# Kernel optimization log

Hardware: AMD Instinct MI355X
Metric: run time of the kernel (lower is better)

## Reference

```python
import jax, jax.numpy as jnp
import numpy as np

B, NQ, NKV = 16, 4096, 77
QUERY_DIM, CONTEXT_DIM = 320, 768
HEADS, DIM_HEAD = 8, 64
INNER = HEADS * DIM_HEAD
SCALE = DIM_HEAD ** (-0.5)
MAX_NEG = -jnp.finfo(jnp.float32).max / 2


def setup_inputs() -> dict:
    key = jax.random.key(0)
    ks = jax.random.split(key, 8)
    x = jax.random.normal(ks[0], (B, NQ, QUERY_DIM), dtype=jnp.float32)
    context = jax.random.normal(ks[1], (B, NKV, CONTEXT_DIM), dtype=jnp.float32)
    mask = jax.random.randint(ks[2], (B, 1, 1, NKV), 0, 2).astype(bool)
    s = 0.02
    Wq = jax.random.normal(ks[3], (QUERY_DIM, INNER), dtype=jnp.float32) * s
    Wk = jax.random.normal(ks[4], (CONTEXT_DIM, INNER), dtype=jnp.float32) * s
    Wv = jax.random.normal(ks[5], (CONTEXT_DIM, INNER), dtype=jnp.float32) * s
    Wo = jax.random.normal(ks[6], (INNER, QUERY_DIM), dtype=jnp.float32) * s
    bo = jnp.zeros((QUERY_DIM,), dtype=jnp.float32)
    return {"x": x, "context": context, "mask": mask,
            "Wq": Wq, "Wk": Wk, "Wv": Wv, "Wo": Wo, "bo": bo}


def reference(x, context, mask, Wq, Wk, Wv, Wo, bo):
    # projections (bias-free Linears)
    q = (x @ Wq).reshape(B, NQ, HEADS, DIM_HEAD)        # b q h d
    k = (context @ Wk).reshape(B, NKV, HEADS, DIM_HEAD)  # b k h d
    v = (context @ Wv).reshape(B, NKV, HEADS, DIM_HEAD)  # b k h d
    # additive mask bias: 0 where mask, -finfo.max/2 where ~mask (matches masked_fill_)
    bias = jnp.where(mask, jnp.float32(0), MAX_NEG)      # broadcast to b h q k
    sim = jnp.einsum('bqhd,bkhd->bhqk', q, k) * SCALE + bias
    attn = jax.nn.softmax(sim, axis=-1)
    out = jnp.einsum('bhqk,bkhd->bqhd', attn, v).reshape(B, NQ, INNER)
    return out @ Wo + bo  # dropout p=0 -> identity
```

## Files before the change

kernel.cpp:

```cpp
#include <hip/hip_runtime.h>

typedef unsigned short ushort_t;
typedef __attribute__((ext_vector_type(8))) short bf16x8;
typedef __attribute__((ext_vector_type(4))) float f32x4;

#define B_SZ   16
#define NQ     4096
#define NKV    77
#define QDIM   320
#define CDIM   768
#define HEADS  8
#define DHEAD  64
#define INNER  512
#define M_ROWS (B_SZ * NQ)
#define VT_STR 104

__device__ __forceinline__ ushort_t f2bf(float f) {
  unsigned u = __builtin_bit_cast(unsigned, f);
  u = (u + 0x7fffu + ((u >> 16) & 1u)) >> 16;
  return (ushort_t)u;
}

__device__ __forceinline__ void async16(const ushort_t* g, ushort_t* l) {
  __builtin_amdgcn_global_load_lds(
      (const __attribute__((address_space(1))) unsigned int*)g,
      (__attribute__((address_space(3))) unsigned int*)l,
      16, 0, 0);
}

__global__ void mask_bias_kernel(const unsigned char* __restrict__ mraw,
                                 float* __restrict__ biasT) {
  __shared__ int s_u8, s_w4;
  if (threadIdx.x == 0) { s_u8 = 0; s_w4 = 0; }
  __syncthreads();
  const int nbytes = B_SZ * NKV;
  for (int i = threadIdx.x; i < nbytes; i += blockDim.x) {
    unsigned char v = mraw[i];
    if (v && (i & 3)) atomicOr(&s_u8, 1);
    if (v && ((i & 7) == 4)) atomicOr(&s_w4, 1);
  }
  __syncthreads();
  int mode = s_u8 ? 0 : (s_w4 ? 1 : 2);
  for (int i = threadIdx.x; i < B_SZ * 80; i += blockDim.x) {
    int b = i / 80, kv = i - b * 80;
    float bias = -2e30f;
    if (kv < NKV) {
      int idx = b * NKV + kv;
      long long m;
      if (mode == 0)      m = (long long)mraw[idx];
      else if (mode == 1) m = (long long)((const int*)mraw)[idx];
      else                m = ((const long long*)mraw)[idx];
      bias = m ? 0.0f : -1e30f;
    }
    biasT[i] = bias;
  }
}

__global__ void cast_f32_bf16(const float* __restrict__ in,
                              ushort_t* __restrict__ out, int n4) {
  int i = blockIdx.x * blockDim.x + threadIdx.x;
  int stride = gridDim.x * blockDim.x;
  const float4* in4 = (const float4*)in;
  ushort4* out4 = (ushort4*)out;
  for (; i < n4; i += stride) {
    float4 v = in4[i];
    ushort4 o;
    o.x = f2bf(v.x); o.y = f2bf(v.y); o.z = f2bf(v.z); o.w = f2bf(v.w);
    out4[i] = o;
  }
}

__global__ void tcast_f32_bf16(const float* __restrict__ in,
                               ushort_t* __restrict__ out,
                               int K, int N, int Npad, float scale) {
  int i = blockIdx.x * blockDim.x + threadIdx.x;
  int stride = gridDim.x * blockDim.x;
  int total = Npad * K;
  for (; i < total; i += stride) {
    int n = i / K, k = i - n * K;
    out[i] = (n < N) ? f2bf(in[(size_t)k * N + n] * scale) : (ushort_t)0;
  }
}

__global__ void vtrans_kernel(const ushort_t* __restrict__ kvb,
                              ushort_t* __restrict__ vt) {
  const int h = blockIdx.y, b = blockIdx.z;
  const int wid = threadIdx.x >> 6, lane = threadIdx.x & 63;
  const int d = blockIdx.x * 4 + wid;
  ushort_t* dst = vt + (size_t)(b * HEADS + h) * (64 * VT_STR) + d * VT_STR;
  for (int kv = lane; kv < VT_STR; kv += 64)
    dst[kv] = (kv < NKV)
        ? kvb[(size_t)(b * NKV + kv) * 1024 + 512 + h * 64 + d]
        : (ushort_t)0;
}

__global__ __launch_bounds__(256) void gemm_bf16(
    const ushort_t* __restrict__ A, const ushort_t* __restrict__ Bt,
    ushort_t* __restrict__ Cb,
    int K, int Astride, int Bstride, int Cstride) {
  __shared__ ushort_t As[128 * 64];
  __shared__ ushort_t Bs[128 * 64];
  const int tid = threadIdx.x;
  const int wid = tid >> 6, lane = tid & 63;
  const int wr = wid >> 1, wc = wid & 1;
  const int tileM = blockIdx.x * 128, tileN = blockIdx.y * 128;

  f32x4 acc[4][4];
#pragma unroll
  for (int m = 0; m < 4; ++m)
#pragma unroll
    for (int n = 0; n < 4; ++n) acc[m][n] = (f32x4){0.f, 0.f, 0.f, 0.f};

  const int srow = lane >> 3;
  const int scol = (lane & 7) * 8;

  for (int kt = 0; kt < K; kt += 64) {
    __syncthreads();
#pragma unroll
    for (int j = 0; j < 4; ++j) {
      int s = wid * 4 + j;
      const ushort_t* ga = A + (size_t)(tileM + s * 8 + srow) * Astride + kt + scol;
      const ushort_t* gb = Bt + (size_t)(tileN + s * 8 + srow) * Bstride + kt + scol;
      async16(ga, As + s * 512);
      async16(gb, Bs + s * 512);
    }
    __syncthreads();
#pragma unroll
    for (int kc = 0; kc < 2; ++kc) {
      bf16x8 af[4], bfr[4];
#pragma unroll
      for (int m = 0; m < 4; ++m)
        af[m] = *(const bf16x8*)&As[(wr * 64 + m * 16 + (lane & 15)) * 64 + kc * 32 + (lane >> 4) * 8];
#pragma unroll
      for (int n = 0; n < 4; ++n)
        bfr[n] = *(const bf16x8*)&Bs[(wc * 64 + n * 16 + (lane & 15)) * 64 + kc * 32 + (lane >> 4) * 8];
#pragma unroll
      for (int m = 0; m < 4; ++m)
#pragma unroll
        for (int n = 0; n < 4; ++n)
          acc[m][n] = __builtin_amdgcn_mfma_f32_16x16x32_bf16(af[m], bfr[n], acc[m][n], 0, 0, 0);
    }
  }

  const int r0 = tileM + wr * 64;
  const int c0 = tileN + wc * 64;
  const int rl2 = (lane >> 4) * 4;
  const int cl = lane & 15;
#pragma unroll
  for (int m = 0; m < 4; ++m)
#pragma unroll
    for (int n = 0; n < 4; ++n) {
      int col = c0 + n * 16 + cl;
#pragma unroll
      for (int r = 0; r < 4; ++r)
        Cb[(size_t)(r0 + m * 16 + rl2 + r) * Cstride + col] = f2bf(acc[m][n][r]);
    }
}

__global__ __launch_bounds__(256, 2) void gemm_qproj_ws(
    const float* __restrict__ x, const ushort_t* __restrict__ Wt,
    ushort_t* __restrict__ qb) {
  __shared__ __align__(16) float As[32 * 320];
  const int tid = threadIdx.x, wid = tid >> 6, lane = tid & 63;
  const int rl = lane & 15, g = lane >> 4;
  const int nbase = blockIdx.y * 128 + wid * 32;
  const size_t Mbase = (size_t)blockIdx.x * 128;

  bf16x8 bf[2][10];
#pragma unroll
  for (int n = 0; n < 2; ++n)
#pragma unroll
    for (int kc = 0; kc < 10; ++kc)
      bf[n][kc] = *(const bf16x8*)&Wt[(size_t)(nbase + n * 16 + rl) * QDIM + kc * 32 + g * 8];

  unsigned off[10];
#pragma unroll
  for (int i = 0; i < 10; ++i) {
    unsigned p = wid * 10240 + i * 1024 + lane * 16;
    unsigned row = p / 1280u;
    unsigned rem = p - row * 1280u;
    off[i] = (unsigned)((Mbase + row) * 1280u) + (rem ^ ((row & 7u) << 4));
  }

  const char* xB = (const char*)x;
  char* AsB = (char*)As;

  for (int it = 0; it < 4; ++it) {
#pragma unroll
    for (int i = 0; i < 10; ++i)
      async16((const ushort_t*)(xB + off[i]),
              (ushort_t*)(AsB + wid * 10240 + i * 1024));
    __syncthreads();

    f32x4 acc[2][2];
#pragma unroll
    for (int m = 0; m < 2; ++m)
#pragma unroll
      for (int n = 0; n < 2; ++n) acc[m][n] = (f32x4){0.f, 0.f, 0.f, 0.f};

#pragma unroll
    for (int kc = 0; kc < 10; ++kc) {
      bf16x8 af[2];
#pragma unroll
      for (int m = 0; m < 2; ++m) {
        const int row = m * 16 + rl;
        const int cb = kc * 128 + g * 32;
        const int s = (row & 7) << 4;
        f32x4 lo = *(const f32x4*)(AsB + row * 1280 + (cb ^ s));
        f32x4 hi = *(const f32x4*)(AsB + row * 1280 + ((cb + 16) ^ s));
        unsigned w0, w1, w2, w3;
        asm("v_cvt_pk_bf16_f32 %0, %1, %2" : "=v"(w0) : "v"(lo[0]), "v"(lo[1]));
        asm("v_cvt_pk_bf16_f32 %0, %1, %2" : "=v"(w1) : "v"(lo[2]), "v"(lo[3]));
        asm("v_cvt_pk_bf16_f32 %0, %1, %2" : "=v"(w2) : "v"(hi[0]), "v"(hi[1]));
        asm("v_cvt_pk_bf16_f32 %0, %1, %2" : "=v"(w3) : "v"(hi[2]), "v"(hi[3]));
        union { unsigned u[4]; bf16x8 v; } cv;
        cv.u[0] = w0; cv.u[1] = w1; cv.u[2] = w2; cv.u[3] = w3;
        af[m] = cv.v;
      }
#pragma unroll
      for (int m = 0; m < 2; ++m)
#pragma unroll
        for (int n = 0; n < 2; ++n)
          acc[m][n] = __builtin_amdgcn_mfma_f32_16x16x32_bf16(af[m], bf[n][kc], acc[m][n], 0, 0, 0);
    }

    const size_t r0 = Mbase + it * 32;
#pragma unroll
    for (int m = 0; m < 2; ++m)
#pragma unroll
      for (int n = 0; n < 2; ++n) {
        const int col = nbase + n * 16 + rl;
#pragma unroll
        for (int r = 0; r < 4; ++r)
          qb[(r0 + m * 16 + g * 4 + r) * INNER + col] = f2bf(acc[m][n][r]);
      }

    if (it < 3) {
      __syncthreads();
#pragma unroll
      for (int i = 0; i < 10; ++i) off[i] += 32 * 1280;
    }
  }
}

__global__ __launch_bounds__(512, 2) void gemm_oproj(
    const ushort_t* __restrict__ A, const ushort_t* __restrict__ Wt,
    const float* __restrict__ bo, float* __restrict__ out) {
  __shared__ ushort_t As[2][128 * 64];
  __shared__ ushort_t Bs[2][384 * 64];
  const int tid = threadIdx.x;
  const int wid = tid >> 6, lane = tid & 63;
  const int wr = wid & 1, wc = wid >> 1;
  const int rl = lane & 15, kh = (lane >> 4) * 8;
  const int tileM = blockIdx.x * 128;

  f32x4 acc[4][6];
#pragma unroll
  for (int m = 0; m < 4; ++m)
#pragma unroll
    for (int n = 0; n < 6; ++n) acc[m][n] = (f32x4){0.f, 0.f, 0.f, 0.f};

#define OP_STAGE(BUF, KT)                                                     \
  _Pragma("unroll")                                                           \
  for (int i = 0; i < 2; ++i) {                                               \
    int chunk = tid + i * 512;                                                \
    int row = chunk >> 3, c8 = chunk & 7;                                     \
    async16(A + (size_t)(tileM + row) * INNER + (KT) + c8 * 8,                \
            &As[BUF][chunk * 8]);                                             \
  }                                                                           \
  _Pragma("unroll")                                                           \
  for (int i = 0; i < 6; ++i) {                                               \
    int chunk = tid + i * 512;                                                \
    int n = chunk >> 3, c8 = chunk & 7;                                       \
    async16(Wt + (size_t)n * INNER + (KT) + c8 * 8, &Bs[BUF][chunk * 8]);     \
  }

  OP_STAGE(0, 0)
  __syncthreads();

  for (int s = 0; s < 8; ++s) {
    const int cur = s & 1;
    if (s < 7) { OP_STAGE(cur ^ 1, (s + 1) * 64) }
#pragma unroll
    for (int kc = 0; kc < 2; ++kc) {
      bf16x8 af[4], bfr[6];
#pragma unroll
      for (int m = 0; m < 4; ++m)
        af[m] = *(const bf16x8*)&As[cur][(wr * 64 + m * 16 + rl) * 64 + kc * 32 + kh];
#pragma unroll
      for (int n = 0; n < 6; ++n)
        bfr[n] = *(const bf16x8*)&Bs[cur][(wc * 96 + n * 16 + rl) * 64 + kc * 32 + kh];
#pragma unroll
      for (int m = 0; m < 4; ++m)
#pragma unroll
        for (int n = 0; n < 6; ++n)
          acc[m][n] = __builtin_amdgcn_mfma_f32_16x16x32_bf16(af[m], bfr[n], acc[m][n], 0, 0, 0);
    }
    __syncthreads();
  }

  const int r0 = tileM + wr * 64;
  const int c0 = wc * 96;
  const int rl2 = (lane >> 4) * 4, cl = lane & 15;
#pragma unroll
  for (int n = 0; n < 6; ++n) {
    int col = c0 + n * 16 + cl;
    if (col < QDIM) {
      float bv = bo[col];
#pragma unroll
      for (int m = 0; m < 4; ++m)
#pragma unroll
        for (int r = 0; r < 4; ++r)
          out[(size_t)(r0 + m * 16 + rl2 + r) * QDIM + col] = acc[m][n][r] + bv;
    }
  }
}

__global__ __launch_bounds__(256) void attn_kernel(
    const ushort_t* __restrict__ qb, const ushort_t* __restrict__ kvb,
    const ushort_t* __restrict__ vt, const float* __restrict__ biasT,
    ushort_t* __restrict__ ab) {
  __shared__ ushort_t Vt[64 * VT_STR];
  __shared__ ushort_t P[4 * 16 * VT_STR];
  const int qt = blockIdx.x, h = blockIdx.y, b = blockIdx.z;
  const int tid = threadIdx.x, wid = tid >> 6, lane = tid & 63;
  const int rl = lane & 15;
  const int kh = (lane >> 4) * 8;

  const ushort_t* vtg = vt + (size_t)(b * HEADS + h) * (64 * VT_STR);
  for (int i = tid; i < 832; i += 256) async16(vtg + i * 8, Vt + i * 8);
  for (int i = tid; i < 832; i += 256)
    *(bf16x8*)&P[i * 8] = (bf16x8){0, 0, 0, 0, 0, 0, 0, 0};

  bf16x8 kf[5][2];
  float bias_v[5];
#pragma unroll
  for (int nt = 0; nt < 5; ++nt) {
    int kv = nt * 16 + rl;
    bias_v[nt] = biasT[b * 80 + kv];
    kf[nt][0] = (bf16x8){0, 0, 0, 0, 0, 0, 0, 0};
    kf[nt][1] = (bf16x8){0, 0, 0, 0, 0, 0, 0, 0};
    if (kv < NKV) {
      const ushort_t* kp = &kvb[(size_t)(b * NKV + kv) * 1024 + h * 64 + kh];
      kf[nt][0] = *(const bf16x8*)kp;
      kf[nt][1] = *(const bf16x8*)(kp + 32);
    }
  }
  __syncthreads();

  const int qbase = b * NQ + qt * 256;
  const int pbase = wid * (16 * VT_STR);
#pragma unroll 1
  for (int chunk = 0; chunk < 4; ++chunk) {
    if (chunk) __syncthreads();
    const int row0 = chunk * 64 + wid * 16;

    const ushort_t* qp = &qb[(size_t)(qbase + row0 + rl) * INNER + h * 64 + kh];
    bf16x8 qf0 = *(const bf16x8*)qp;
    bf16x8 qf1 = *(const bf16x8*)(qp + 32);

    f32x4 s[5];
#pragma unroll
    for (int nt = 0; nt < 5; ++nt) {
      s[nt] = (f32x4){0.f, 0.f, 0.f, 0.f};
      s[nt] = __builtin_amdgcn_mfma_f32_16x16x32_bf16(qf0, kf[nt][0], s[nt], 0, 0, 0);
      s[nt] = __builtin_amdgcn_mfma_f32_16x16x32_bf16(qf1, kf[nt][1], s[nt], 0, 0, 0);
    }

    float mx[4] = {-3.0e38f, -3.0e38f, -3.0e38f, -3.0e38f};
#pragma unroll
    for (int nt = 0; nt < 5; ++nt)
#pragma unroll
      for (int r = 0; r < 4; ++r) {
        float v = s[nt][r] + bias_v[nt];
        s[nt][r] = v;
        mx[r] = fmaxf(mx[r], v);
      }
#pragma unroll
    for (int d = 1; d < 16; d <<= 1)
#pragma unroll
      for (int r = 0; r < 4; ++r) mx[r] = fmaxf(mx[r], __shfl_xor(mx[r], d, 64));

    float sm[4] = {0.f, 0.f, 0.f, 0.f};
#pragma unroll
    for (int nt = 0; nt < 5; ++nt)
#pragma unroll
      for (int r = 0; r < 4; ++r) {
        float p = __expf(s[nt][r] - mx[r]);
        s[nt][r] = p;
        sm[r] += p;
      }
#pragma unroll
    for (int d = 1; d < 16; d <<= 1)
#pragma unroll
      for (int r = 0; r < 4; ++r) sm[r] += __shfl_xor(sm[r], d, 64);

    float rcp[4];
#pragma unroll
    for (int r = 0; r < 4; ++r) rcp[r] = 1.0f / sm[r];

#pragma unroll
    for (int nt = 0; nt < 5; ++nt)
#pragma unroll
      for (int r = 0; r < 4; ++r)
        P[pbase + ((lane >> 4) * 4 + r) * VT_STR + nt * 16 + rl] = f2bf(s[nt][r]);

    f32x4 o[4];
#pragma unroll
    for (int n = 0; n < 4; ++n) o[n] = (f32x4){0.f, 0.f, 0.f, 0.f};
#pragma unroll
    for (int kc = 0; kc < 3; ++kc) {
      bf16x8 pf = *(const bf16x8*)&P[pbase + rl * VT_STR + kc * 32 + kh];
#pragma unroll
      for (int n = 0; n < 4; ++n) {
        bf16x8 vf = *(const bf16x8*)&Vt[(n * 16 + rl) * VT_STR + kc * 32 + kh];
        o[n] = __builtin_amdgcn_mfma_f32_16x16x32_bf16(pf, vf, o[n], 0, 0, 0);
      }
    }

#pragma unroll
    for (int n = 0; n < 4; ++n)
#pragma unroll
      for (int r = 0; r < 4; ++r)
        P[pbase + ((lane >> 4) * 4 + r) * VT_STR + n * 16 + rl] = f2bf(o[n][r] * rcp[r]);

    __syncthreads();

    {
      const int rflat = tid >> 2, d0 = (tid & 3) * 16;
      const ushort_t* src = &P[(rflat >> 4) * (16 * VT_STR) + (rflat & 15) * VT_STR + d0];
      ushort_t* dst = &ab[(size_t)(qbase + chunk * 64 + rflat) * INNER + h * 64 + d0];
      *(bf16x8*)dst = *(const bf16x8*)src;
      *(bf16x8*)(dst + 8) = *(const bf16x8*)(src + 8);
    }
  }
}

extern "C" void kernel_launch(void* const* d_in, const int* in_sizes, int n_in,
                              void* d_out, int out_size, void* d_ws, size_t ws_size,
                              hipStream_t stream) {
  (void)in_sizes; (void)n_in; (void)out_size; (void)ws_size;
  const float* x   = (const float*)d_in[0];
  const float* ctx = (const float*)d_in[1];
  const unsigned char* mask = (const unsigned char*)d_in[2];
  const float* Wq = (const float*)d_in[3];
  const float* Wk = (const float*)d_in[4];
  const float* Wv = (const float*)d_in[5];
  const float* Wo = (const float*)d_in[6];
  const float* bo = (const float*)d_in[7];
  float* out = (float*)d_out;

  char* ws = (char*)d_ws;
  size_t off = 0;
  auto alloc = [&](size_t bytes) {
    char* p = ws + off;
    off += (bytes + 255) & ~(size_t)255;
    return p;
  };
  float*    biasT = (float*)alloc(B_SZ * 80 * sizeof(float));
  ushort_t* ab    = (ushort_t*)alloc((size_t)M_ROWS * INNER * 2);
  ushort_t* qb    = (ushort_t*)alloc((size_t)M_ROWS * INNER * 2);
  ushort_t* cb    = (ushort_t*)alloc((size_t)1280 * CDIM * 2);
  ushort_t* Wqb   = (ushort_t*)alloc((size_t)INNER * QDIM * 2);
  ushort_t* Wkvb  = (ushort_t*)alloc((size_t)1024 * CDIM * 2);
  ushort_t* Wob   = (ushort_t*)alloc((size_t)384 * INNER * 2);
  ushort_t* kvb   = (ushort_t*)alloc((size_t)1280 * 1024 * 2);
  ushort_t* vt    = (ushort_t*)alloc((size_t)B_SZ * HEADS * 64 * VT_STR * 2);

  mask_bias_kernel<<<1, 256, 0, stream>>>(mask, biasT);
  cast_f32_bf16<<<512, 256, 0, stream>>>(ctx, cb, B_SZ * NKV * CDIM / 4);
  tcast_f32_bf16<<<640, 256, 0, stream>>>(Wq, Wqb, QDIM, INNER, INNER, 0.125f);
  tcast_f32_bf16<<<1536, 256, 0, stream>>>(Wk, Wkvb, CDIM, INNER, INNER, 1.0f);
  tcast_f32_bf16<<<1536, 256, 0, stream>>>(Wv, Wkvb + (size_t)INNER * CDIM, CDIM, INNER, INNER, 1.0f);
  tcast_f32_bf16<<<768, 256, 0, stream>>>(Wo, Wob, INNER, QDIM, 384, 1.0f);

  gemm_qproj_ws<<<dim3(M_ROWS / 128, 4), 256, 0, stream>>>(x, Wqb, qb);
  dim3 g2(1280 / 128, 1024 / 128);
  gemm_bf16<<<g2, 256, 0, stream>>>(cb, Wkvb, kvb, CDIM, CDIM, CDIM, 1024);
  vtrans_kernel<<<dim3(16, HEADS, B_SZ), 256, 0, stream>>>(kvb, vt);
  attn_kernel<<<dim3(NQ / 256, HEADS, B_SZ), 256, 0, stream>>>(qb, kvb, vt, biasT, ab);
  gemm_oproj<<<M_ROWS / 128, 512, 0, stream>>>(ab, Wob, bo, out);
}
```

Measured before the change: 210.6 us.

## Rewrite Q and output projection GEMMs with triple-buffered async LDS pipelines

The Q projection now uses 512-thread blocks that each cover a full 128x512 output tile. It streams x and Wq in K-chunks through a three-stage async global-to-LDS pipeline with explicit vmcnt waits and swizzled layouts, and stages the bf16 results through LDS so they can be written to global memory in coalesced 16-byte chunks. The output projection gets a similar three-stage pipeline with 32-wide K steps and XOR-swizzled LDS, replacing its previous double buffer. The aim is to hide global-load latency, avoid LDS bank conflicts and re-read x only once per tile. In exchange, large dynamic shared memory allocations (144KB and 96KB) reduce occupancy, and it relies on hand-tuned vmcnt counts.

New measurement: 190.8 us. -9.4%, faster.

```diff
diff --git a/kernel.cpp b/kernel.cpp
--- a/kernel.cpp
+++ b/kernel.cpp
@@ -27,6 +27,8 @@
       (__attribute__((address_space(3))) unsigned int*)l,
       16, 0, 0);
 }
+
+#define VMCNT(N) asm volatile("s_waitcnt vmcnt(" #N ")" ::: "memory")
 
 __global__ void mask_bias_kernel(const unsigned char* __restrict__ mraw,
                                  float* __restrict__ biasT) {
@@ -157,102 +159,142 @@
     }
 }
 
-__global__ __launch_bounds__(256, 2) void gemm_qproj_ws(
+__global__ __launch_bounds__(512, 2) void gemm_qproj_p(
     const float* __restrict__ x, const ushort_t* __restrict__ Wt,
     ushort_t* __restrict__ qb) {
-  __shared__ __align__(16) float As[32 * 320];
+  extern __shared__ char sm[];
   const int tid = threadIdx.x, wid = tid >> 6, lane = tid & 63;
   const int rl = lane & 15, g = lane >> 4;
-  const int nbase = blockIdx.y * 128 + wid * 32;
+  const int wr = wid & 1, wc = wid >> 1;
   const size_t Mbase = (size_t)blockIdx.x * 128;
 
-  bf16x8 bf[2][10];
-#pragma unroll
-  for (int n = 0; n < 2; ++n)
-#pragma unroll
-    for (int kc = 0; kc < 10; ++kc)
-      bf[n][kc] = *(const bf16x8*)&Wt[(size_t)(nbase + n * 16 + rl) * QDIM + kc * 32 + g * 8];
-
-  unsigned off[10];
-#pragma unroll
-  for (int i = 0; i < 10; ++i) {
-    unsigned p = wid * 10240 + i * 1024 + lane * 16;
-    unsigned row = p / 1280u;
-    unsigned rem = p - row * 1280u;
-    off[i] = (unsigned)((Mbase + row) * 1280u) + (rem ^ ((row & 7u) << 4));
-  }
-
+  size_t asrc[2]; unsigned adst[2];
+#pragma unroll
+  for (int i = 0; i < 2; ++i) {
+    int c = tid + i * 512, row = c >> 3, c16 = c & 7;
+    asrc[i] = (Mbase + row) * 1280 + (unsigned)((c16 * 16) ^ ((row & 7) << 4));
+    adst[i] = c * 16;
+  }
+  size_t bsrc[4]; unsigned bdst[4];
+#pragma unroll
+  for (int i = 0; i < 4; ++i) {
+    int c = tid + i * 512, row = c >> 2, c16 = c & 3;
+    bsrc[i] = (size_t)row * 640 + (unsigned)((c16 * 16) ^ ((row & 3) << 4));
+    bdst[i] = 16384 + c * 16;
+  }
   const char* xB = (const char*)x;
-  char* AsB = (char*)As;
-
-  for (int it = 0; it < 4; ++it) {
-#pragma unroll
-    for (int i = 0; i < 10; ++i)
-      async16((const ushort_t*)(xB + off[i]),
-              (ushort_t*)(AsB + wid * 10240 + i * 1024));
+  const char* WtB = (const char*)Wt;
+
+  f32x4 acc[4][8];
+#pragma unroll
+  for (int m = 0; m < 4; ++m)
+#pragma unroll
+    for (int n = 0; n < 8; ++n) acc[m][n] = (f32x4){0.f, 0.f, 0.f, 0.f};
+
+#define QSTAGE(K)                                                           \
+  {                                                                         \
+    char* bb = sm + (unsigned)((K) % 3) * 49152u;                           \
+    _Pragma("unroll")                                                       \
+    for (int i = 0; i < 2; ++i)                                             \
+      async16((const ushort_t*)(xB + asrc[i] + (size_t)(K) * 128),          \
+              (ushort_t*)(bb + adst[i]));                                   \
+    _Pragma("unroll")                                                       \
+    for (int i = 0; i < 4; ++i)                                             \
+      async16((const ushort_t*)(WtB + bsrc[i] + (size_t)(K) * 64),          \
+              (ushort_t*)(bb + bdst[i]));                                   \
+  }
+
+  QSTAGE(0)
+  QSTAGE(1)
+  for (int s = 0; s < 10; ++s) {
+    if (s < 8) QSTAGE(s + 2)
+    if (s < 8)       { VMCNT(12); }
+    else if (s == 8) { VMCNT(6); }
+    else             { VMCNT(0); }
+    __builtin_amdgcn_sched_barrier(0);
+    __builtin_amdgcn_s_barrier();
+    __builtin_amdgcn_sched_barrier(0);
+
+    const char* Ab = sm + (unsigned)(s % 3) * 49152u;
+    const char* Bb = Ab + 16384;
+    bf16x8 af[4], bfr[8];
+#pragma unroll
+    for (int m = 0; m < 4; ++m) {
+      const int row = wr * 64 + m * 16 + rl;
+      const int sw = (row & 7) << 4;
+      f32x4 lo = *(const f32x4*)(Ab + row * 128 + ((g * 32) ^ sw));
+      f32x4 hi = *(const f32x4*)(Ab + row * 128 + ((g * 32 + 16) ^ sw));
+      unsigned w0, w1, w2, w3;
+      asm("v_cvt_pk_bf16_f32 %0, %1, %2" : "=v"(w0) : "v"(lo[0]), "v"(lo[1]));
+      asm("v_cvt_pk_bf16_f32 %0, %1, %2" : "=v"(w1) : "v"(lo[2]), "v"(lo[3]));
+      asm("v_cvt_pk_bf16_f32 %0, %1, %2" : "=v"(w2) : "v"(hi[0]), "v"(hi[1]));
+      asm("v_cvt_pk_bf16_f32 %0, %1, %2" : "=v"(w3) : "v"(hi[2]), "v"(hi[3]));
+      union { unsigned u[4]; bf16x8 v; } cv;
+      cv.u[0] = w0; cv.u[1] = w1; cv.u[2] = w2; cv.u[3] = w3;
+      af[m] = cv.v;
+    }
+#pragma unroll
+    for (int n = 0; n < 8; ++n) {
+      const int row = wc * 128 + n * 16 + rl;
+      bfr[n] = *(const bf16x8*)(Bb + row * 64 + ((g * 16) ^ ((row & 3) << 4)));
+    }
+#pragma unroll
+    for (int m = 0; m < 4; ++m)
+#pragma unroll
+      for (int n = 0; n < 8; ++n)
+        acc[m][n] = __builtin_amdgcn_mfma_f32_16x16x32_bf16(af[m], bfr[n], acc[m][n], 0, 0, 0);
+    __builtin_amdgcn_sched_barrier(0);
+    __builtin_amdgcn_s_barrier();
+    __builtin_amdgcn_sched_barrier(0);
+  }
+
+  ushort_t* eb = (ushort_t*)sm;
+#pragma unroll
+  for (int h = 0; h < 2; ++h) {
+    if (h) __syncthreads();
+    if (wr == h) {
+#pragma unroll
+      for (int m = 0; m < 4; ++m)
+#pragma unroll
+        for (int n = 0; n < 8; ++n)
+#pragma unroll
+          for (int r = 0; r < 4; ++r)
+            eb[(m * 16 + g * 4 + r) * 512 + wc * 128 + n * 16 + rl] = f2bf(acc[m][n][r]);
+    }
     __syncthreads();
-
-    f32x4 acc[2][2];
-#pragma unroll
-    for (int m = 0; m < 2; ++m)
-#pragma unroll
-      for (int n = 0; n < 2; ++n) acc[m][n] = (f32x4){0.f, 0.f, 0.f, 0.f};
-
-#pragma unroll
-    for (int kc = 0; kc < 10; ++kc) {
-      bf16x8 af[2];
-#pragma unroll
-      for (int m = 0; m < 2; ++m) {
-        const int row = m * 16 + rl;
-        const int cb = kc * 128 + g * 32;
-        const int s = (row & 7) << 4;
-        f32x4 lo = *(const f32x4*)(AsB + row * 1280 + (cb ^ s));
-        f32x4 hi = *(const f32x4*)(AsB + row * 1280 + ((cb + 16) ^ s));
-        unsigned w0, w1, w2, w3;
-        asm("v_cvt_pk_bf16_f32 %0, %1, %2" : "=v"(w0) : "v"(lo[0]), "v"(lo[1]));
-        asm("v_cvt_pk_bf16_f32 %0, %1, %2" : "=v"(w1) : "v"(lo[2]), "v"(lo[3]));
-        asm("v_cvt_pk_bf16_f32 %0, %1, %2" : "=v"(w2) : "v"(hi[0]), "v"(hi[1]));
-        asm("v_cvt_pk_bf16_f32 %0, %1, %2" : "=v"(w3) : "v"(hi[2]), "v"(hi[3]));
-        union { unsigned u[4]; bf16x8 v; } cv;
-        cv.u[0] = w0; cv.u[1] = w1; cv.u[2] = w2; cv.u[3] = w3;
-        af[m] = cv.v;
-      }
-#pragma unroll
-      for (int m = 0; m < 2; ++m)
-#pragma unroll
-        for (int n = 0; n < 2; ++n)
-          acc[m][n] = __builtin_amdgcn_mfma_f32_16x16x32_bf16(af[m], bf[n][kc], acc[m][n], 0, 0, 0);
-    }
-
-    const size_t r0 = Mbase + it * 32;
-#pragma unroll
-    for (int m = 0; m < 2; ++m)
-#pragma unroll
-      for (int n = 0; n < 2; ++n) {
-        const int col = nbase + n * 16 + rl;
-#pragma unroll
-        for (int r = 0; r < 4; ++r)
-          qb[(r0 + m * 16 + g * 4 + r) * INNER + col] = f2bf(acc[m][n][r]);
-      }
-
-    if (it < 3) {
-      __syncthreads();
-#pragma unroll
-      for (int i = 0; i < 10; ++i) off[i] += 32 * 1280;
-    }
-  }
-}
-
-__global__ __launch_bounds__(512, 2) void gemm_oproj(
+#pragma unroll
+    for (int i = 0; i < 8; ++i) {
+      int c = tid + i * 512, row = c >> 6;
+      *(bf16x8*)(qb + (Mbase + h * 64 + row) * 512 + (c & 63) * 8) =
+          *(const bf16x8*)(eb + c * 8);
+    }
+  }
+}
+
+__global__ __launch_bounds__(512, 2) void gemm_oproj_p(
     const ushort_t* __restrict__ A, const ushort_t* __restrict__ Wt,
     const float* __restrict__ bo, float* __restrict__ out) {
-  __shared__ ushort_t As[2][128 * 64];
-  __shared__ ushort_t Bs[2][384 * 64];
-  const int tid = threadIdx.x;
-  const int wid = tid >> 6, lane = tid & 63;
+  extern __shared__ char sm[];
+  const int tid = threadIdx.x, wid = tid >> 6, lane = tid & 63;
+  const int rl = lane & 15, g = lane >> 4;
   const int wr = wid & 1, wc = wid >> 1;
-  const int rl = lane & 15, kh = (lane >> 4) * 8;
-  const int tileM = blockIdx.x * 128;
+  const size_t Mbase = (size_t)blockIdx.x * 128;
+
+  size_t asrc; unsigned adst;
+  {
+    int c = tid, row = c >> 2, c16 = c & 3;
+    asrc = (Mbase + row) * 1024 + (unsigned)((c16 * 16) ^ ((row & 3) << 4));
+    adst = c * 16;
+  }
+  size_t bsrc[3]; unsigned bdst[3];
+#pragma unroll
+  for (int i = 0; i < 3; ++i) {
+    int c = tid + i * 512, row = c >> 2, c16 = c & 3;
+    bsrc[i] = (size_t)row * 1024 + (unsigned)((c16 * 16) ^ ((row & 3) << 4));
+    bdst[i] = 8192 + c * 16;
+  }
+  const char* AB = (const char*)A;
+  const char* WtB = (const char*)Wt;
 
   f32x4 acc[4][6];
 #pragma unroll
@@ -260,58 +302,63 @@
 #pragma unroll
     for (int n = 0; n < 6; ++n) acc[m][n] = (f32x4){0.f, 0.f, 0.f, 0.f};
 
-#define OP_STAGE(BUF, KT)                                                     \
-  _Pragma("unroll")                                                           \
-  for (int i = 0; i < 2; ++i) {                                               \
-    int chunk = tid + i * 512;                                                \
-    int row = chunk >> 3, c8 = chunk & 7;                                     \
-    async16(A + (size_t)(tileM + row) * INNER + (KT) + c8 * 8,                \
-            &As[BUF][chunk * 8]);                                             \
-  }                                                                           \
-  _Pragma("unroll")                                                           \
-  for (int i = 0; i < 6; ++i) {                                               \
-    int chunk = tid + i * 512;                                                \
-    int n = chunk >> 3, c8 = chunk & 7;                                       \
-    async16(Wt + (size_t)n * INNER + (KT) + c8 * 8, &Bs[BUF][chunk * 8]);     \
-  }
-
-  OP_STAGE(0, 0)
-  __syncthreads();
-
-  for (int s = 0; s < 8; ++s) {
-    const int cur = s & 1;
-    if (s < 7) { OP_STAGE(cur ^ 1, (s + 1) * 64) }
-#pragma unroll
-    for (int kc = 0; kc < 2; ++kc) {
-      bf16x8 af[4], bfr[6];
-#pragma unroll
-      for (int m = 0; m < 4; ++m)
-        af[m] = *(const bf16x8*)&As[cur][(wr * 64 + m * 16 + rl) * 64 + kc * 32 + kh];
+#define OSTAGE(K)                                                           \
+  {                                                                         \
+    char* bb = sm + (unsigned)((K) % 3) * 32768u;                           \
+    async16((const ushort_t*)(AB + asrc + (size_t)(K) * 64),                \
+            (ushort_t*)(bb + adst));                                        \
+    _Pragma("unroll")                                                       \
+    for (int i = 0; i < 3; ++i)                                             \
+      async16((const ushort_t*)(WtB + bsrc[i] + (size_t)(K) * 64),          \
+              (ushort_t*)(bb + bdst[i]));                                   \
+  }
+
+  OSTAGE(0)
+  OSTAGE(1)
+  for (int s = 0; s < 16; ++s) {
+    if (s < 14) OSTAGE(s + 2)
+    if (s < 14)       { VMCNT(8); }
+    else if (s == 14) { VMCNT(4); }
+    else              { VMCNT(0); }
+    __builtin_amdgcn_sched_barrier(0);
+    __builtin_amdgcn_s_barrier();
+    __builtin_amdgcn_sched_barrier(0);
+
+    const char* Ab = sm + (unsigned)(s % 3) * 32768u;
+    const char* Bb = Ab + 8192;
+    bf16x8 af[4], bfr[6];
+#pragma unroll
+    for (int m = 0; m < 4; ++m) {
+      const int row = wr * 64 + m * 16 + rl;
+      af[m] = *(const bf16x8*)(Ab + row * 64 + ((g * 16) ^ ((row & 3) << 4)));
+    }
+#pragma unroll
+    for (int n = 0; n < 6; ++n) {
+      const int row = wc * 96 + n * 16 + rl;
+      bfr[n] = *(const bf16x8*)(Bb + row * 64 + ((g * 16) ^ ((row & 3) << 4)));
+    }
+#pragma unroll
+    for (int m = 0; m < 4; ++m)
 #pragma unroll
       for (int n = 0; n < 6; ++n)
-        bfr[n] = *(const bf16x8*)&Bs[cur][(wc * 96 + n * 16 + rl) * 64 + kc * 32 + kh];
-#pragma unroll
-      for (int m = 0; m < 4; ++m)
-#pragma unroll
-        for (int n = 0; n < 6; ++n)
-          acc[m][n] = __builtin_amdgcn_mfma_f32_16x16x32_bf16(af[m], bfr[n], acc[m][n], 0, 0, 0);
-    }
-    __syncthreads();
-  }
-
-  const int r0 = tileM + wr * 64;
+        acc[m][n] = __builtin_amdgcn_mfma_f32_16x16x32_bf16(af[m], bfr[n], acc[m][n], 0, 0, 0);
+    __builtin_amdgcn_sched_barrier(0);
+    __builtin_amdgcn_s_barrier();
+    __builtin_amdgcn_sched_barrier(0);
+  }
+
+  const size_t r0 = Mbase + wr * 64;
   const int c0 = wc * 96;
-  const int rl2 = (lane >> 4) * 4, cl = lane & 15;
 #pragma unroll
   for (int n = 0; n < 6; ++n) {
-    int col = c0 + n * 16 + cl;
+    int col = c0 + n * 16 + rl;
     if (col < QDIM) {
       float bv = bo[col];
 #pragma unroll
       for (int m = 0; m < 4; ++m)
 #pragma unroll
         for (int r = 0; r < 4; ++r)
-          out[(size_t)(r0 + m * 16 + rl2 + r) * QDIM + col] = acc[m][n][r] + bv;
+          out[(r0 + m * 16 + g * 4 + r) * QDIM + col] = acc[m][n][r] + bv;
     }
   }
 }
@@ -381,23 +428,23 @@
 #pragma unroll
       for (int r = 0; r < 4; ++r) mx[r] = fmaxf(mx[r], __shfl_xor(mx[r], d, 64));
 
-    float sm[4] = {0.f, 0.f, 0.f, 0.f};
+    float sm_[4] = {0.f, 0.f, 0.f, 0.f};
 #pragma unroll
     for (int nt = 0; nt < 5; ++nt)
 #pragma unroll
       for (int r = 0; r < 4; ++r) {
         float p = __expf(s[nt][r] - mx[r]);
         s[nt][r] = p;
-        sm[r] += p;
+        sm_[r] += p;
       }
 #pragma unroll
     for (int d = 1; d < 16; d <<= 1)
 #pragma unroll
-      for (int r = 0; r < 4; ++r) sm[r] += __shfl_xor(sm[r], d, 64);
+      for (int r = 0; r < 4; ++r) sm_[r] += __shfl_xor(sm_[r], d, 64);
 
     float rcp[4];
 #pragma unroll
-    for (int r = 0; r < 4; ++r) rcp[r] = 1.0f / sm[r];
+    for (int r = 0; r < 4; ++r) rcp[r] = 1.0f / sm_[r];
 
 #pragma unroll
     for (int nt = 0; nt < 5; ++nt)
@@ -449,6 +496,11 @@
   const float* Wo = (const float*)d_in[6];
   const float* bo = (const float*)d_in[7];
   float* out = (float*)d_out;
+
+  hipFuncSetAttribute((const void*)gemm_qproj_p,
+                      hipFuncAttributeMaxDynamicSharedMemorySize, 147456);
+  hipFuncSetAttribute((const void*)gemm_oproj_p,
+                      hipFuncAttributeMaxDynamicSharedMemorySize, 98304);
 
   char* ws = (char*)d_ws;
   size_t off = 0;
@@ -474,10 +526,10 @@
   tcast_f32_bf16<<<1536, 256, 0, stream>>>(Wv, Wkvb + (size_t)INNER * CDIM, CDIM, INNER, INNER, 1.0f);
   tcast_f32_bf16<<<768, 256, 0, stream>>>(Wo, Wob, INNER, QDIM, 384, 1.0f);
 
-  gemm_qproj_ws<<<dim3(M_ROWS / 128, 4), 256, 0, stream>>>(x, Wqb, qb);
+  gemm_qproj_p<<<M_ROWS / 128, 512, 147456, stream>>>(x, Wqb, qb);
   dim3 g2(1280 / 128, 1024 / 128);
   gemm_bf16<<<g2, 256, 0, stream>>>(cb, Wkvb, kvb, CDIM, CDIM, CDIM, 1024);
   vtrans_kernel<<<dim3(16, HEADS, B_SZ), 256, 0, stream>>>(kvb, vt);
   attn_kernel<<<dim3(NQ / 256, HEADS, B_SZ), 256, 0, stream>>>(qb, kvb, vt, biasT, ab);
-  gemm_oproj<<<M_ROWS / 128, 512, 0, stream>>>(ab, Wob, bo, out);
-}
+  gemm_oproj_p<<<M_ROWS / 128, 512, 98304, stream>>>(ab, Wob, bo, out);
+}
```

## Restructure Q and output projections into single-shot 64-row tiles with LDS-staged epilogue

Applied to the files above, without the earlier changes.

The Q projection now loads a 64x320 fp32 tile of x into LDS once, computes all 512 output columns per block with 8 waves, and stages results through LDS so global stores are coalesced 16-byte writes. The output projection loads the whole 64x512 A tile into swizzled LDS in one shot and reads Wo fragments directly from global/L2 instead of double-buffering both operands through LDS. Both cut per-block synchronisation and redundant A loads, at the cost of large dynamic LDS (80KB/64KB) per block, which may limit occupancy, and more global B-fragment traffic.

Result: slower. 293.9 us (+39.6%).

```diff
diff --git a/kernel.cpp b/kernel.cpp
--- a/kernel.cpp
+++ b/kernel.cpp
@@ -157,161 +157,133 @@
     }
 }
 
-__global__ __launch_bounds__(256, 2) void gemm_qproj_ws(
+__global__ __launch_bounds__(512, 2) void gemm_qproj_v3(
     const float* __restrict__ x, const ushort_t* __restrict__ Wt,
     ushort_t* __restrict__ qb) {
-  __shared__ __align__(16) float As[32 * 320];
+  extern __shared__ char sm[];
   const int tid = threadIdx.x, wid = tid >> 6, lane = tid & 63;
   const int rl = lane & 15, g = lane >> 4;
-  const int nbase = blockIdx.y * 128 + wid * 32;
-  const size_t Mbase = (size_t)blockIdx.x * 128;
-
-  bf16x8 bf[2][10];
-#pragma unroll
-  for (int n = 0; n < 2; ++n)
-#pragma unroll
-    for (int kc = 0; kc < 10; ++kc)
-      bf[n][kc] = *(const bf16x8*)&Wt[(size_t)(nbase + n * 16 + rl) * QDIM + kc * 32 + g * 8];
-
-  unsigned off[10];
+  const int wr = wid & 1, wc = wid >> 1;
+  const size_t Mbase = (size_t)blockIdx.x * 64;
+  const char* xB = (const char*)x;
+
 #pragma unroll
   for (int i = 0; i < 10; ++i) {
-    unsigned p = wid * 10240 + i * 1024 + lane * 16;
-    unsigned row = p / 1280u;
-    unsigned rem = p - row * 1280u;
-    off[i] = (unsigned)((Mbase + row) * 1280u) + (rem ^ ((row & 7u) << 4));
-  }
-
-  const char* xB = (const char*)x;
-  char* AsB = (char*)As;
-
-  for (int it = 0; it < 4; ++it) {
-#pragma unroll
-    for (int i = 0; i < 10; ++i)
-      async16((const ushort_t*)(xB + off[i]),
-              (ushort_t*)(AsB + wid * 10240 + i * 1024));
-    __syncthreads();
-
-    f32x4 acc[2][2];
+    unsigned c = tid + i * 512;
+    unsigned row = c / 80u, c16 = c - row * 80u;
+    size_t src = (Mbase + row) * 1280 + (size_t)((c16 ^ (row & 7u)) * 16);
+    async16((const ushort_t*)(xB + src), (ushort_t*)(sm + c * 16));
+  }
+  __syncthreads();
+
+  f32x4 acc[2][8];
+#pragma unroll
+  for (int m = 0; m < 2; ++m)
+#pragma unroll
+    for (int n = 0; n < 8; ++n) acc[m][n] = (f32x4){0.f, 0.f, 0.f, 0.f};
+
+#pragma unroll
+  for (int kc = 0; kc < 10; ++kc) {
+    bf16x8 bfr[8];
+#pragma unroll
+    for (int n = 0; n < 8; ++n)
+      bfr[n] = *(const bf16x8*)&Wt[(size_t)(wc * 128 + n * 16 + rl) * QDIM + kc * 32 + g * 8];
+    bf16x8 af[2];
+#pragma unroll
+    for (int m = 0; m < 2; ++m) {
+      const int row = wr * 32 + m * 16 + rl;
+      const int sw = (row & 7) << 4;
+      f32x4 lo = *(const f32x4*)(sm + row * 1280 + ((kc * 128 + g * 32) ^ sw));
+      f32x4 hi = *(const f32x4*)(sm + row * 1280 + ((kc * 128 + g * 32 + 16) ^ sw));
+      unsigned w0, w1, w2, w3;
+      asm("v_cvt_pk_bf16_f32 %0, %1, %2" : "=v"(w0) : "v"(lo[0]), "v"(lo[1]));
+      asm("v_cvt_pk_bf16_f32 %0, %1, %2" : "=v"(w1) : "v"(lo[2]), "v"(lo[3]));
+      asm("v_cvt_pk_bf16_f32 %0, %1, %2" : "=v"(w2) : "v"(hi[0]), "v"(hi[1]));
+      asm("v_cvt_pk_bf16_f32 %0, %1, %2" : "=v"(w3) : "v"(hi[2]), "v"(hi[3]));
+      union { unsigned u[4]; bf16x8 v; } cv;
+      cv.u[0] = w0; cv.u[1] = w1; cv.u[2] = w2; cv.u[3] = w3;
+      af[m] = cv.v;
+    }
 #pragma unroll
     for (int m = 0; m < 2; ++m)
 #pragma unroll
-      for (int n = 0; n < 2; ++n) acc[m][n] = (f32x4){0.f, 0.f, 0.f, 0.f};
-
-#pragma unroll
-    for (int kc = 0; kc < 10; ++kc) {
-      bf16x8 af[2];
-#pragma unroll
-      for (int m = 0; m < 2; ++m) {
-        const int row = m * 16 + rl;
-        const int cb = kc * 128 + g * 32;
-        const int s = (row & 7) << 4;
-        f32x4 lo = *(const f32x4*)(AsB + row * 1280 + (cb ^ s));
-        f32x4 hi = *(const f32x4*)(AsB + row * 1280 + ((cb + 16) ^ s));
-        unsigned w0, w1, w2, w3;
-        asm("v_cvt_pk_bf16_f32 %0, %1, %2" : "=v"(w0) : "v"(lo[0]), "v"(lo[1]));
-        asm("v_cvt_pk_bf16_f32 %0, %1, %2" : "=v"(w1) : "v"(lo[2]), "v"(lo[3]));
-        asm("v_cvt_pk_bf16_f32 %0, %1, %2" : "=v"(w2) : "v"(hi[0]), "v"(hi[1]));
-        asm("v_cvt_pk_bf16_f32 %0, %1, %2" : "=v"(w3) : "v"(hi[2]), "v"(hi[3]));
-        union { unsigned u[4]; bf16x8 v; } cv;
-        cv.u[0] = w0; cv.u[1] = w1; cv.u[2] = w2; cv.u[3] = w3;
-        af[m] = cv.v;
-      }
-#pragma unroll
-      for (int m = 0; m < 2; ++m)
-#pragma unroll
-        for (int n = 0; n < 2; ++n)
-          acc[m][n] = __builtin_amdgcn_mfma_f32_16x16x32_bf16(af[m], bf[n][kc], acc[m][n], 0, 0, 0);
-    }
-
-    const size_t r0 = Mbase + it * 32;
-#pragma unroll
-    for (int m = 0; m < 2; ++m)
-#pragma unroll
-      for (int n = 0; n < 2; ++n) {
-        const int col = nbase + n * 16 + rl;
-#pragma unroll
-        for (int r = 0; r < 4; ++r)
-          qb[(r0 + m * 16 + g * 4 + r) * INNER + col] = f2bf(acc[m][n][r]);
-      }
-
-    if (it < 3) {
-      __syncthreads();
-#pragma unroll
-      for (int i = 0; i < 10; ++i) off[i] += 32 * 1280;
-    }
-  }
-}
-
-__global__ __launch_bounds__(512, 2) void gemm_oproj(
+      for (int n = 0; n < 8; ++n)
+        acc[m][n] = __builtin_amdgcn_mfma_f32_16x16x32_bf16(af[m], bfr[n], acc[m][n], 0, 0, 0);
+  }
+
+  __syncthreads();
+  ushort_t* eb = (ushort_t*)sm;
+#pragma unroll
+  for (int m = 0; m < 2; ++m)
+#pragma unroll
+    for (int n = 0; n < 8; ++n)
+#pragma unroll
+      for (int r = 0; r < 4; ++r)
+        eb[(wr * 32 + m * 16 + g * 4 + r) * 528 + wc * 128 + n * 16 + rl] = f2bf(acc[m][n][r]);
+  __syncthreads();
+#pragma unroll
+  for (int i = 0; i < 8; ++i) {
+    unsigned flat = tid + i * 512;
+    unsigned row = flat >> 6, c8 = flat & 63;
+    *(bf16x8*)(qb + (Mbase + row) * INNER + c8 * 8) =
+        *(const bf16x8*)(sm + row * 1056 + c8 * 16);
+  }
+}
+
+__global__ __launch_bounds__(512, 2) void gemm_oproj_v3(
     const ushort_t* __restrict__ A, const ushort_t* __restrict__ Wt,
     const float* __restrict__ bo, float* __restrict__ out) {
-  __shared__ ushort_t As[2][128 * 64];
-  __shared__ ushort_t Bs[2][384 * 64];
-  const int tid = threadIdx.x;
-  const int wid = tid >> 6, lane = tid & 63;
+  extern __shared__ char sm[];
+  const int tid = threadIdx.x, wid = tid >> 6, lane = tid & 63;
+  const int rl = lane & 15, g = lane >> 4;
   const int wr = wid & 1, wc = wid >> 1;
-  const int rl = lane & 15, kh = (lane >> 4) * 8;
-  const int tileM = blockIdx.x * 128;
-
-  f32x4 acc[4][6];
-#pragma unroll
-  for (int m = 0; m < 4; ++m)
+  const size_t Mbase = (size_t)blockIdx.x * 64;
+  const char* AB = (const char*)A;
+
+#pragma unroll
+  for (int i = 0; i < 8; ++i) {
+    unsigned c = tid + i * 512;
+    unsigned row = c >> 6, c16 = c & 63;
+    size_t src = (Mbase + row) * 1024 + (size_t)((c16 ^ (row & 7u)) * 16);
+    async16((const ushort_t*)(AB + src), (ushort_t*)(sm + c * 16));
+  }
+  __syncthreads();
+
+  f32x4 acc[2][6];
+#pragma unroll
+  for (int m = 0; m < 2; ++m)
 #pragma unroll
     for (int n = 0; n < 6; ++n) acc[m][n] = (f32x4){0.f, 0.f, 0.f, 0.f};
 
-#define OP_STAGE(BUF, KT)                                                     \
-  _Pragma("unroll")                                                           \
-  for (int i = 0; i < 2; ++i) {                                               \
-    int chunk = tid + i * 512;                                                \
-    int row = chunk >> 3, c8 = chunk & 7;                                     \
-    async16(A + (size_t)(tileM + row) * INNER + (KT) + c8 * 8,                \
-            &As[BUF][chunk * 8]);                                             \
-  }                                                                           \
-  _Pragma("unroll")                                                           \
-  for (int i = 0; i < 6; ++i) {                                               \
-    int chunk = tid + i * 512;                                                \
-    int n = chunk >> 3, c8 = chunk & 7;                                       \
-    async16(Wt + (size_t)n * INNER + (KT) + c8 * 8, &Bs[BUF][chunk * 8]);     \
-  }
-
-  OP_STAGE(0, 0)
-  __syncthreads();
-
-  for (int s = 0; s < 8; ++s) {
-    const int cur = s & 1;
-    if (s < 7) { OP_STAGE(cur ^ 1, (s + 1) * 64) }
-#pragma unroll
-    for (int kc = 0; kc < 2; ++kc) {
-      bf16x8 af[4], bfr[6];
-#pragma unroll
-      for (int m = 0; m < 4; ++m)
-        af[m] = *(const bf16x8*)&As[cur][(wr * 64 + m * 16 + rl) * 64 + kc * 32 + kh];
+#pragma unroll 4
+  for (int kc = 0; kc < 16; ++kc) {
+    bf16x8 bfr[6];
+#pragma unroll
+    for (int n = 0; n < 6; ++n)
+      bfr[n] = *(const bf16x8*)&Wt[(size_t)(wc * 96 + n * 16 + rl) * INNER + kc * 32 + g * 8];
+    bf16x8 af[2];
+#pragma unroll
+    for (int m = 0; m < 2; ++m) {
+      const int row = wr * 32 + m * 16 + rl;
+      af[m] = *(const bf16x8*)(sm + row * 1024 + ((kc * 64 + g * 16) ^ ((row & 7) << 4)));
+    }
+#pragma unroll
+    for (int m = 0; m < 2; ++m)
 #pragma unroll
       for (int n = 0; n < 6; ++n)
-        bfr[n] = *(const bf16x8*)&Bs[cur][(wc * 96 + n * 16 + rl) * 64 + kc * 32 + kh];
-#pragma unroll
-      for (int m = 0; m < 4; ++m)
-#pragma unroll
-        for (int n = 0; n < 6; ++n)
-          acc[m][n] = __builtin_amdgcn_mfma_f32_16x16x32_bf16(af[m], bfr[n], acc[m][n], 0, 0, 0);
-    }
-    __syncthreads();
-  }
-
-  const int r0 = tileM + wr * 64;
-  const int c0 = wc * 96;
-  const int rl2 = (lane >> 4) * 4, cl = lane & 15;
+        acc[m][n] = __builtin_amdgcn_mfma_f32_16x16x32_bf16(af[m], bfr[n], acc[m][n], 0, 0, 0);
+  }
+
 #pragma unroll
   for (int n = 0; n < 6; ++n) {
-    int col = c0 + n * 16 + cl;
+    int col = wc * 96 + n * 16 + rl;
     if (col < QDIM) {
       float bv = bo[col];
 #pragma unroll
-      for (int m = 0; m < 4; ++m)
+      for (int m = 0; m < 2; ++m)
 #pragma unroll
         for (int r = 0; r < 4; ++r)
-          out[(size_t)(r0 + m * 16 + rl2 + r) * QDIM + col] = acc[m][n][r] + bv;
+          out[(Mbase + wr * 32 + m * 16 + g * 4 + r) * QDIM + col] = acc[m][n][r] + bv;
     }
   }
 }
@@ -381,23 +353,23 @@
 #pragma unroll
       for (int r = 0; r < 4; ++r) mx[r] = fmaxf(mx[r], __shfl_xor(mx[r], d, 64));
 
-    float sm[4] = {0.f, 0.f, 0.f, 0.f};
+    float sm_[4] = {0.f, 0.f, 0.f, 0.f};
 #pragma unroll
     for (int nt = 0; nt < 5; ++nt)
 #pragma unroll
       for (int r = 0; r < 4; ++r) {
         float p = __expf(s[nt][r] - mx[r]);
         s[nt][r] = p;
-        sm[r] += p;
+        sm_[r] += p;
       }
 #pragma unroll
     for (int d = 1; d < 16; d <<= 1)
 #pragma unroll
-      for (int r = 0; r < 4; ++r) sm[r] += __shfl_xor(sm[r], d, 64);
+      for (int r = 0; r < 4; ++r) sm_[r] += __shfl_xor(sm_[r], d, 64);
 
     float rcp[4];
 #pragma unroll
-    for (int r = 0; r < 4; ++r) rcp[r] = 1.0f / sm[r];
+    for (int r = 0; r < 4; ++r) rcp[r] = 1.0f / sm_[r];
 
 #pragma unroll
     for (int nt = 0; nt < 5; ++nt)
@@ -449,6 +421,11 @@
   const float* Wo = (const float*)d_in[6];
   const float* bo = (const float*)d_in[7];
   float* out = (float*)d_out;
+
+  hipFuncSetAttribute((const void*)gemm_qproj_v3,
+                      hipFuncAttributeMaxDynamicSharedMemorySize, 81920);
+  hipFuncSetAttribute((const void*)gemm_oproj_v3,
+                      hipFuncAttributeMaxDynamicSharedMemorySize, 65536);
 
   char* ws = (char*)d_ws;
   size_t off = 0;
@@ -474,10 +451,10 @@
   tcast_f32_bf16<<<1536, 256, 0, stream>>>(Wv, Wkvb + (size_t)INNER * CDIM, CDIM, INNER, INNER, 1.0f);
   tcast_f32_bf16<<<768, 256, 0, stream>>>(Wo, Wob, INNER, QDIM, 384, 1.0f);
 
-  gemm_qproj_ws<<<dim3(M_ROWS / 128, 4), 256, 0, stream>>>(x, Wqb, qb);
+  gemm_qproj_v3<<<M_ROWS / 64, 512, 81920, stream>>>(x, Wqb, qb);
   dim3 g2(1280 / 128, 1024 / 128);
   gemm_bf16<<<g2, 256, 0, stream>>>(cb, Wkvb, kvb, CDIM, CDIM, CDIM, 1024);
   vtrans_kernel<<<dim3(16, HEADS, B_SZ), 256, 0, stream>>>(kvb, vt);
   attn_kernel<<<dim3(NQ / 256, HEADS, B_SZ), 256, 0, stream>>>(qb, kvb, vt, biasT, ab);
-  gemm_oproj<<<M_ROWS / 128, 512, 0, stream>>>(ab, Wob, bo, out);
-}
+  gemm_oproj_v3<<<M_ROWS / 64, 512, 65536, stream>>>(ab, Wob, bo, out);
+}
```
